# Performance work log

Measured on AMD Instinct MI355X. Metric: run time of the kernel, lower is better.

## Reference

```python
import jax, jax.numpy as jnp
import numpy as np

N_NODES = 100000
N_EDGES = 1600000
C_IN = 128
C_OUT = 64
BN_EPS = 1e-5
LEAKY_SLOPE = 0.01


def setup_inputs() -> dict:
    key = jax.random.key(0)
    k1, k2, k3 = jax.random.split(key, 3)
    x = jax.random.normal(k1, (N_NODES, C_IN), dtype=jnp.float32)
    edge_index = jax.random.randint(k2, (2, N_EDGES), 0, N_NODES, dtype=jnp.int32)
    W = jax.random.normal(k3, (C_IN, C_OUT), dtype=jnp.float32) * (1.0 / np.sqrt(C_IN))
    b = jnp.zeros((C_OUT,), dtype=jnp.float32)
    gamma = jnp.ones((C_OUT,), dtype=jnp.float32)
    beta = jnp.zeros((C_OUT,), dtype=jnp.float32)
    return {"x": x, "edge_index": edge_index, "W": W, "b": b, "gamma": gamma, "beta": beta}


def reference(x, edge_index, W, b, gamma, beta):
    n = x.shape[0]
    # --- GCNConv: add self-loops, symmetric normalization ---
    loop = jnp.arange(n, dtype=edge_index.dtype)
    row = jnp.concatenate([edge_index[0], loop])  # source
    col = jnp.concatenate([edge_index[1], loop])  # target
    deg = jax.ops.segment_sum(jnp.ones_like(col, dtype=x.dtype), col, num_segments=n)
    deg_inv_sqrt = jnp.where(deg > 0, jax.lax.rsqrt(deg), 0.0)
    norm = deg_inv_sqrt[row] * deg_inv_sqrt[col]  # [E+N]
    xw = x @ W  # [N, C_OUT] - transform before aggregation (PyG GCNConv)
    msgs = xw[row] * norm[:, None]  # [E+N, C_OUT]
    out = jax.ops.segment_sum(msgs, col, num_segments=n) + b  # [N, C_OUT]
    # --- BatchNorm (training mode: batch stats over nodes, biased var) ---
    mean = jnp.mean(out, axis=0)
    var = jnp.mean(jnp.square(out - mean), axis=0)
    y = gamma * (out - mean) * jax.lax.rsqrt(var + BN_EPS) + beta
    # --- LeakyReLU (default negative_slope=0.01); dropout p=0 is identity ---
    return jnp.where(y >= 0, y, LEAKY_SLOPE * y)
```

## Files before the change

### kernel.cpp

```cpp
#include <hip/hip_runtime.h>

#define C_IN 128
#define C_OUT 64
#define BN_EPS 1e-5f
#define LEAKY 0.01f

#define BSZ   256
#define NBMAX 512
#define CAP   6144
#define CHUNKA 2048

using bf16x8 = __attribute__((ext_vector_type(8))) __bf16;
using f32x4  = __attribute__((ext_vector_type(4))) float;

__device__ inline unsigned short f2b(float f) {
    unsigned u = __float_as_uint(f);
    return (unsigned short)((u + 0x7fffu + ((u >> 16) & 1u)) >> 16);
}
__device__ inline float b2f(unsigned short b) {
    return __uint_as_float(((unsigned)b) << 16);
}

__global__ __launch_bounds__(256) void k_prep(const float* __restrict__ W,
                                              unsigned short* __restrict__ wb,
                                              int* __restrict__ bfill,
                                              float* __restrict__ stats) {
    int idx = blockIdx.x * 256 + threadIdx.x;
    if (idx < NBMAX) bfill[idx] = 0;
    if (idx >= NBMAX && idx < NBMAX + 2 * C_OUT) stats[idx - NBMAX] = 0.f;
    if (idx >= C_IN * C_OUT) return;
    int k = idx >> 6, col = idx & 63;
    int t = col >> 4, nlo = col & 15;
    int c = k >> 5, q = (k >> 3) & 3, j = k & 7;
    wb[(size_t)((((t * 4 + c) * 4 + q) * 16) + nlo) * 8 + j] = f2b(W[idx]);
}

__global__ __launch_bounds__(256) void k_binA(const int* __restrict__ rows,
                                              const int* __restrict__ cols,
                                              int* __restrict__ bfill,
                                              unsigned* __restrict__ pairs,
                                              int nE, int NB) {
    __shared__ int hist[NBMAX];
    __shared__ int base[NBMAX];
    __shared__ int lstart[NBMAX];
    __shared__ int cursor[NBMAX];
    __shared__ unsigned lpair[CHUNKA];
    __shared__ unsigned short lbkt[CHUNKA];
    __shared__ unsigned lsorted[CHUNKA];
    __shared__ unsigned short lsbkt[CHUNKA];
    int t = threadIdx.x;
    int chunk = blockIdx.x * CHUNKA;
    int cnt = min(chunk + CHUNKA, nE) - chunk;

    hist[t] = 0; hist[t + 256] = 0;
    __syncthreads();

    for (int i = t; i < cnt; i += 256) {
        int c = cols[chunk + i];
        unsigned r = (unsigned)rows[chunk + i];
        int b = c >> 8;
        lpair[i] = ((unsigned)(c & (BSZ - 1)) << 24) | r;
        lbkt[i] = (unsigned short)b;
        atomicAdd(&hist[b], 1);
    }
    __syncthreads();

    int h0 = hist[t], h1 = hist[t + 256];
    if (t < NB && h0) base[t] = atomicAdd(&bfill[t], h0);
    if (t + 256 < NB && h1) base[t + 256] = atomicAdd(&bfill[t + 256], h1);
    lstart[t] = h0; lstart[t + 256] = h1;
    __syncthreads();
    for (int off = 1; off < 512; off <<= 1) {
        int a = (t >= off) ? lstart[t - off] : 0;
        int bb = lstart[t + 256 - off];
        __syncthreads();
        lstart[t] += a; lstart[t + 256] += bb;
        __syncthreads();
    }
    int s0 = lstart[t] - h0, s1 = lstart[t + 256] - h1;
    lstart[t] = s0; lstart[t + 256] = s1;
    cursor[t] = s0; cursor[t + 256] = s1;
    __syncthreads();

    for (int i = t; i < cnt; i += 256) {
        int b = lbkt[i];
        int pos = atomicAdd(&cursor[b], 1);
        lsorted[pos] = lpair[i];
        lsbkt[pos] = (unsigned short)b;
    }
    __syncthreads();

    for (int i = t; i < cnt; i += 256) {
        int b = lsbkt[i];
        int off = base[b] + (i - lstart[b]);
        if (off < CAP)
            pairs[(size_t)b * CAP + off] = lsorted[i];
    }
}

__global__ __launch_bounds__(256) void k_binB(const int* __restrict__ bfill,
                                              const unsigned* __restrict__ pairs,
                                              int2* __restrict__ pd,
                                              int* __restrict__ srcs, int n) {
    __shared__ unsigned rowbuf[CAP];
    __shared__ int sorted[CAP];
    __shared__ int histL[BSZ];
    __shared__ int scanL[BSZ];
    int b = blockIdx.x;
    int t = threadIdx.x;
    int cnt = min(bfill[b], CAP);
    const unsigned* reg = pairs + (size_t)b * CAP;

    histL[t] = 0;
    __syncthreads();
    for (int i = t; i < cnt; i += 256) {
        unsigned p = reg[i];
        rowbuf[i] = p;
        atomicAdd(&histL[p >> 24], 1);
    }
    __syncthreads();

    int hv = histL[t];
    scanL[t] = hv;
    __syncthreads();
    for (int off = 1; off < 256; off <<= 1) {
        int x = (t >= off) ? scanL[t - off] : 0;
        __syncthreads();
        scanL[t] += x;
        __syncthreads();
    }
    int my_start = scanL[t] - hv;

    int s0 = b * CAP;
    int node = (b << 8) + t;
    if (node < n) pd[node] = make_int2(s0 + my_start, hv);
    __syncthreads();
    histL[t] = my_start;
    __syncthreads();
    for (int i = t; i < cnt; i += 256) {
        unsigned p = rowbuf[i];
        int pos = atomicAdd(&histL[p >> 24], 1);
        sorted[pos] = (int)(p & 0xFFFFFFu);
    }
    __syncthreads();
    for (int i = t; i < cnt; i += 256)
        srcs[s0 + i] = sorted[i];
}

__global__ __launch_bounds__(256) void k_gemm(const float* __restrict__ x,
                                              const unsigned short* __restrict__ wb,
                                              const int2* __restrict__ pd,
                                              unsigned short* __restrict__ xwsb, int n) {
    const int lane = threadIdx.x & 63;
    const int wave = threadIdx.x >> 6;
    const int base = (blockIdx.x * 4 + wave) * 16;
    if (base >= n) return;

    const int nlo  = lane & 15;
    const int quad = lane >> 4;

    const bf16x8* Wv = (const bf16x8*)wb;
    bf16x8 Bf[4][4];
    #pragma unroll
    for (int t = 0; t < 4; ++t)
        #pragma unroll
        for (int c = 0; c < 4; ++c)
            Bf[t][c] = Wv[((t * 4 + c) * 4 + quad) * 16 + nlo];

    f32x4 acc[4] = {};
    int m = base + nlo;
    const float* xrow = x + (size_t)(m < n ? m : n - 1) * C_IN;

    #pragma unroll
    for (int c = 0; c < 4; ++c) {
        float4 a0 = *(const float4*)&xrow[c * 32 + quad * 8];
        float4 a1 = *(const float4*)&xrow[c * 32 + quad * 8 + 4];
        bf16x8 Af;
        Af[0] = (__bf16)a0.x; Af[1] = (__bf16)a0.y;
        Af[2] = (__bf16)a0.z; Af[3] = (__bf16)a0.w;
        Af[4] = (__bf16)a1.x; Af[5] = (__bf16)a1.y;
        Af[6] = (__bf16)a1.z; Af[7] = (__bf16)a1.w;
        #pragma unroll
        for (int t = 0; t < 4; ++t)
            acc[t] = __builtin_amdgcn_mfma_f32_16x16x32_bf16(Af, Bf[t][c], acc[t], 0, 0, 0);
    }

    #pragma unroll
    for (int r = 0; r < 4; ++r) {
        int node = base + quad * 4 + r;
        if (node < n) {
            float dn = rsqrtf((float)(pd[node].y + 1));
            #pragma unroll
            for (int t = 0; t < 4; ++t)
                xwsb[(size_t)node * C_OUT + t * 16 + nlo] = f2b(acc[t][r] * dn);
        }
    }
}

#define ACC8(d) do { \
    acc[0] += __uint_as_float((d).x << 16); \
    acc[1] += __uint_as_float((d).x & 0xffff0000u); \
    acc[2] += __uint_as_float((d).y << 16); \
    acc[3] += __uint_as_float((d).y & 0xffff0000u); \
    acc[4] += __uint_as_float((d).z << 16); \
    acc[5] += __uint_as_float((d).z & 0xffff0000u); \
    acc[6] += __uint_as_float((d).w << 16); \
    acc[7] += __uint_as_float((d).w & 0xffff0000u); } while (0)

__global__ __launch_bounds__(256) void k_gather(const int2* __restrict__ pd,
                                                const int* __restrict__ srcs,
                                                const unsigned short* __restrict__ xwsb,
                                                float* __restrict__ out, int n) {
    int lane = threadIdx.x & 63;
    int wv   = threadIdx.x >> 6;
    int s    = lane & 7;
    int g    = (lane >> 3) & 3;
    int h    = lane >> 5;
    int l32  = lane & 31;
    int c0 = s * 8 + ((lane & 8) ? 4 : 0) + ((lane & 16) ? 2 : 0);
    const uint4* xw16 = (const uint4*)xwsb;

    int node = blockIdx.x * 8 + wv * 2 + h;
    bool active = node < n;

    int2 p = active ? pd[node] : make_int2(0, 0);
    int dg = p.y;
    float dn = rsqrtf((float)(dg + 1));
    unsigned selfu = active ? *(const unsigned*)&xwsb[(size_t)node * C_OUT + c0] : 0u;

    float acc[8] = {0.f, 0.f, 0.f, 0.f, 0.f, 0.f, 0.f, 0.f};

    int sv = (active && l32 < dg) ? srcs[p.x + l32] : 0;
    for (int b2 = 0;;) {
        int m = dg - b2;
        #pragma unroll
        for (int j = 0; j < 8; ++j) {
            int idx = j * 4 + g;
            int src = __shfl(sv, (h << 5) + idx);
            if (idx < m) {
                uint4 d = xw16[((size_t)src << 3) + s];
                ACC8(d);
            }
        }
        b2 += 32;
        if (b2 >= dg) break;
        sv = (l32 < dg - b2) ? srcs[p.x + b2 + l32] : 0;
    }

    #pragma unroll
    for (int k = 0; k < 4; ++k) {
        float send = (lane & 8) ? acc[k] : acc[k + 4];
        float recv = __shfl_xor(send, 8);
        acc[k] = ((lane & 8) ? acc[k + 4] : acc[k]) + recv;
    }
    #pragma unroll
    for (int k = 0; k < 2; ++k) {
        float send = (lane & 16) ? acc[k] : acc[k + 2];
        float recv = __shfl_xor(send, 16);
        acc[k] = ((lane & 16) ? acc[k + 2] : acc[k]) + recv;
    }

    if (active) {
        float v0 = (acc[0] + __uint_as_float(selfu << 16)) * dn;
        float v1 = (acc[1] + __uint_as_float(selfu & 0xffff0000u)) * dn;
        *(float2*)&out[(size_t)node * C_OUT + c0] = make_float2(v0, v1);
    }
}

__global__ __launch_bounds__(256) void k_stats(const float* __restrict__ agg,
                                               float* __restrict__ stats, int n) {
    int c = threadIdx.x & 63;
    int sub = threadIdx.x >> 6;
    float s = 0.f, s2 = 0.f;
    for (int node = blockIdx.x * 4 + sub; node < n; node += gridDim.x * 4) {
        float v = agg[(size_t)node * C_OUT + c];
        s += v;
        s2 += v * v;
    }
    __shared__ float red[2][4][64];
    red[0][sub][c] = s;
    red[1][sub][c] = s2;
    __syncthreads();
    if (sub == 0) {
        s  = red[0][0][c] + red[0][1][c] + red[0][2][c] + red[0][3][c];
        s2 = red[1][0][c] + red[1][1][c] + red[1][2][c] + red[1][3][c];
        atomicAdd(&stats[c], s);
        atomicAdd(&stats[64 + c], s2);
    }
}

__global__ __launch_bounds__(256) void k_final(const float* __restrict__ stats,
                                               const float* __restrict__ gamma,
                                               const float* __restrict__ beta,
                                               float* __restrict__ out, int n) {
    int gid = blockIdx.x * 256 + threadIdx.x;
    int total4 = n * (C_OUT / 4);
    if (gid >= total4) return;
    int c4 = (gid & 15) * 4;
    float inv_n = 1.0f / (float)n;
    float4 s  = *(const float4*)&stats[c4];
    float4 s2 = *(const float4*)&stats[64 + c4];
    float4 g4 = *(const float4*)&gamma[c4];
    float4 b4 = *(const float4*)&beta[c4];
    float4 v = ((const float4*)out)[gid];

    float m, var, k, y;
    m = s.x * inv_n; var = s2.x * inv_n - m * m; k = rsqrtf(var + BN_EPS) * g4.x;
    y = (v.x - m) * k + b4.x; v.x = y >= 0.f ? y : LEAKY * y;
    m = s.y * inv_n; var = s2.y * inv_n - m * m; k = rsqrtf(var + BN_EPS) * g4.y;
    y = (v.y - m) * k + b4.y; v.y = y >= 0.f ? y : LEAKY * y;
    m = s.z * inv_n; var = s2.z * inv_n - m * m; k = rsqrtf(var + BN_EPS) * g4.z;
    y = (v.z - m) * k + b4.z; v.z = y >= 0.f ? y : LEAKY * y;
    m = s.w * inv_n; var = s2.w * inv_n - m * m; k = rsqrtf(var + BN_EPS) * g4.w;
    y = (v.w - m) * k + b4.w; v.w = y >= 0.f ? y : LEAKY * y;

    ((float4*)out)[gid] = v;
}

extern "C" void kernel_launch(void* const* d_in, const int* in_sizes, int n_in,
                              void* d_out, int out_size, void* d_ws, size_t ws_size,
                              hipStream_t stream) {
    const float* x     = (const float*)d_in[0];
    const int*   ei    = (const int*)d_in[1];
    const float* W     = (const float*)d_in[2];
    const float* gamma = (const float*)d_in[4];
    const float* beta  = (const float*)d_in[5];
    float* out = (float*)d_out;

    int n  = in_sizes[0] / C_IN;
    int nE = in_sizes[1] / 2;
    const int* rows = ei;
    const int* cols = ei + nE;
    int NB = (n + BSZ - 1) / BSZ;

    int2* pd = (int2*)d_ws;
    unsigned short* xwsb = (unsigned short*)(pd + n);
    unsigned* pairs = (unsigned*)(xwsb + (size_t)n * C_OUT);
    int* srcs = (int*)pairs;
    int* bfill = (int*)(pairs + (size_t)NB * CAP);
    float* stats = (float*)(bfill + NBMAX);
    unsigned short* wb = (unsigned short*)(stats + 2 * C_OUT);

    k_prep<<<(C_IN * C_OUT + 255) / 256, 256, 0, stream>>>(W, wb, bfill, stats);
    k_binA<<<(nE + CHUNKA - 1) / CHUNKA, 256, 0, stream>>>(rows, cols, bfill, pairs, nE, NB);
    k_binB<<<NB, 256, 0, stream>>>(bfill, pairs, pd, srcs, n);
    k_gemm<<<(n + 63) / 64, 256, 0, stream>>>(x, wb, pd, xwsb, n);
    k_gather<<<(n + 7) / 8, 256, 0, stream>>>(pd, srcs, xwsb, out, n);
    k_stats<<<512, 256, 0, stream>>>(out, stats, n);
    k_final<<<(n * (C_OUT / 4) + 255) / 256, 256, 0, stream>>>(stats, gamma, beta, out, n);
}
```

Measured before the change: 216.6 us.

## Fuse BatchNorm statistics into gather and use 16 lanes per node

```diff
diff --git a/kernel.cpp b/kernel.cpp
--- a/kernel.cpp
+++ b/kernel.cpp
@@ -9,6 +9,7 @@
 #define NBMAX 512
 #define CAP   6144
 #define CHUNKA 2048
+#define NPART 16
 
 using bf16x8 = __attribute__((ext_vector_type(8))) __bf16;
 using f32x4  = __attribute__((ext_vector_type(4))) float;
@@ -24,10 +25,10 @@
 __global__ __launch_bounds__(256) void k_prep(const float* __restrict__ W,
                                               unsigned short* __restrict__ wb,
                                               int* __restrict__ bfill,
-                                              float* __restrict__ stats) {
+                                              float* __restrict__ part) {
     int idx = blockIdx.x * 256 + threadIdx.x;
     if (idx < NBMAX) bfill[idx] = 0;
-    if (idx >= NBMAX && idx < NBMAX + 2 * C_OUT) stats[idx - NBMAX] = 0.f;
+    if (idx < NPART * 128) part[idx] = 0.f;
     if (idx >= C_IN * C_OUT) return;
     int k = idx >> 6, col = idx & 63;
     int t = col >> 4, nlo = col & 15;
@@ -210,41 +211,45 @@
 __global__ __launch_bounds__(256) void k_gather(const int2* __restrict__ pd,
                                                 const int* __restrict__ srcs,
                                                 const unsigned short* __restrict__ xwsb,
-                                                float* __restrict__ out, int n) {
+                                                float* __restrict__ out,
+                                                float* __restrict__ part, int n) {
+    __shared__ float sredS[16][64];
+    __shared__ float sredQ[16][64];
     int lane = threadIdx.x & 63;
     int wv   = threadIdx.x >> 6;
     int s    = lane & 7;
-    int g    = (lane >> 3) & 3;
-    int h    = lane >> 5;
-    int l32  = lane & 31;
-    int c0 = s * 8 + ((lane & 8) ? 4 : 0) + ((lane & 16) ? 2 : 0);
+    int g    = (lane >> 3) & 1;
+    int q    = lane >> 4;
+    int l16  = lane & 15;
+    int c0 = s * 8 + ((lane & 8) ? 4 : 0);
     const uint4* xw16 = (const uint4*)xwsb;
 
-    int node = blockIdx.x * 8 + wv * 2 + h;
+    int node = blockIdx.x * 16 + wv * 4 + q;
     bool active = node < n;
 
     int2 p = active ? pd[node] : make_int2(0, 0);
     int dg = p.y;
     float dn = rsqrtf((float)(dg + 1));
-    unsigned selfu = active ? *(const unsigned*)&xwsb[(size_t)node * C_OUT + c0] : 0u;
+    uint2 selfu = active ? *(const uint2*)&xwsb[(size_t)node * C_OUT + c0]
+                         : make_uint2(0u, 0u);
 
     float acc[8] = {0.f, 0.f, 0.f, 0.f, 0.f, 0.f, 0.f, 0.f};
 
-    int sv = (active && l32 < dg) ? srcs[p.x + l32] : 0;
+    int sv = (active && l16 < dg) ? srcs[p.x + l16] : 0;
     for (int b2 = 0;;) {
         int m = dg - b2;
         #pragma unroll
         for (int j = 0; j < 8; ++j) {
-            int idx = j * 4 + g;
-            int src = __shfl(sv, (h << 5) + idx);
+            int idx = j * 2 + g;
+            int src = __shfl(sv, (lane & 48) + idx);
             if (idx < m) {
                 uint4 d = xw16[((size_t)src << 3) + s];
                 ACC8(d);
             }
         }
-        b2 += 32;
+        b2 += 16;
         if (b2 >= dg) break;
-        sv = (l32 < dg - b2) ? srcs[p.x + b2 + l32] : 0;
+        sv = (l16 < dg - b2) ? srcs[p.x + b2 + l16] : 0;
     }
 
     #pragma unroll
@@ -253,65 +258,76 @@
         float recv = __shfl_xor(send, 8);
         acc[k] = ((lane & 8) ? acc[k + 4] : acc[k]) + recv;
     }
-    #pragma unroll
-    for (int k = 0; k < 2; ++k) {
-        float send = (lane & 16) ? acc[k] : acc[k + 2];
-        float recv = __shfl_xor(send, 16);
-        acc[k] = ((lane & 16) ? acc[k + 2] : acc[k]) + recv;
-    }
-
-    if (active) {
-        float v0 = (acc[0] + __uint_as_float(selfu << 16)) * dn;
-        float v1 = (acc[1] + __uint_as_float(selfu & 0xffff0000u)) * dn;
-        *(float2*)&out[(size_t)node * C_OUT + c0] = make_float2(v0, v1);
-    }
-}
-
-__global__ __launch_bounds__(256) void k_stats(const float* __restrict__ agg,
-                                               float* __restrict__ stats, int n) {
-    int c = threadIdx.x & 63;
-    int sub = threadIdx.x >> 6;
-    float s = 0.f, s2 = 0.f;
-    for (int node = blockIdx.x * 4 + sub; node < n; node += gridDim.x * 4) {
-        float v = agg[(size_t)node * C_OUT + c];
-        s += v;
-        s2 += v * v;
-    }
-    __shared__ float red[2][4][64];
-    red[0][sub][c] = s;
-    red[1][sub][c] = s2;
-    __syncthreads();
-    if (sub == 0) {
-        s  = red[0][0][c] + red[0][1][c] + red[0][2][c] + red[0][3][c];
-        s2 = red[1][0][c] + red[1][1][c] + red[1][2][c] + red[1][3][c];
-        atomicAdd(&stats[c], s);
-        atomicAdd(&stats[64 + c], s2);
-    }
-}
-
-__global__ __launch_bounds__(256) void k_final(const float* __restrict__ stats,
+
+    float v0 = active ? (acc[0] + __uint_as_float(selfu.x << 16)) * dn : 0.f;
+    float v1 = active ? (acc[1] + __uint_as_float(selfu.x & 0xffff0000u)) * dn : 0.f;
+    float v2 = active ? (acc[2] + __uint_as_float(selfu.y << 16)) * dn : 0.f;
+    float v3 = active ? (acc[3] + __uint_as_float(selfu.y & 0xffff0000u)) * dn : 0.f;
+
+    if (active)
+        *(float4*)&out[(size_t)node * C_OUT + c0] = make_float4(v0, v1, v2, v3);
+
+    int slot = wv * 4 + q;
+    sredS[slot][c0 + 0] = v0;       sredQ[slot][c0 + 0] = v0 * v0;
+    sredS[slot][c0 + 1] = v1;       sredQ[slot][c0 + 1] = v1 * v1;
+    sredS[slot][c0 + 2] = v2;       sredQ[slot][c0 + 2] = v2 * v2;
+    sredS[slot][c0 + 3] = v3;       sredQ[slot][c0 + 3] = v3 * v3;
+    __syncthreads();
+    int t = threadIdx.x;
+    if (t < 128) {
+        int cc = t & 63;
+        float a = 0.f;
+        if (t < 64) {
+            #pragma unroll
+            for (int j = 0; j < 16; ++j) a += sredS[j][cc];
+        } else {
+            #pragma unroll
+            for (int j = 0; j < 16; ++j) a += sredQ[j][cc];
+        }
+        atomicAdd(&part[(blockIdx.x & (NPART - 1)) * 128 + t], a);
+    }
+}
+
+__global__ __launch_bounds__(256) void k_final(const float* __restrict__ part,
                                                const float* __restrict__ gamma,
                                                const float* __restrict__ beta,
                                                float* __restrict__ out, int n) {
-    int gid = blockIdx.x * 256 + threadIdx.x;
+    __shared__ float lp[NPART * 128];
+    __shared__ float tot[128];
+    int t = threadIdx.x;
+    #pragma unroll
+    for (int r = 0; r < NPART * 128 / 256; ++r)
+        lp[t + r * 256] = part[t + r * 256];
+    __syncthreads();
+    if (t < 128) {
+        float a = 0.f;
+        #pragma unroll
+        for (int j = 0; j < NPART; ++j) a += lp[j * 128 + t];
+        tot[t] = a;
+    }
+    __syncthreads();
+
+    int gid = blockIdx.x * 256 + t;
     int total4 = n * (C_OUT / 4);
     if (gid >= total4) return;
     int c4 = (gid & 15) * 4;
     float inv_n = 1.0f / (float)n;
-    float4 s  = *(const float4*)&stats[c4];
-    float4 s2 = *(const float4*)&stats[64 + c4];
     float4 g4 = *(const float4*)&gamma[c4];
     float4 b4 = *(const float4*)&beta[c4];
     float4 v = ((const float4*)out)[gid];
 
     float m, var, k, y;
-    m = s.x * inv_n; var = s2.x * inv_n - m * m; k = rsqrtf(var + BN_EPS) * g4.x;
+    m = tot[c4 + 0] * inv_n; var = tot[64 + c4 + 0] * inv_n - m * m;
+    k = rsqrtf(var + BN_EPS) * g4.x;
     y = (v.x - m) * k + b4.x; v.x = y >= 0.f ? y : LEAKY * y;
-    m = s.y * inv_n; var = s2.y * inv_n - m * m; k = rsqrtf(var + BN_EPS) * g4.y;
+    m = tot[c4 + 1] * inv_n; var = tot[64 + c4 + 1] * inv_n - m * m;
+    k = rsqrtf(var + BN_EPS) * g4.y;
     y = (v.y - m) * k + b4.y; v.y = y >= 0.f ? y : LEAKY * y;
-    m = s.z * inv_n; var = s2.z * inv_n - m * m; k = rsqrtf(var + BN_EPS) * g4.z;
+    m = tot[c4 + 2] * inv_n; var = tot[64 + c4 + 2] * inv_n - m * m;
+    k = rsqrtf(var + BN_EPS) * g4.z;
     y = (v.z - m) * k + b4.z; v.z = y >= 0.f ? y : LEAKY * y;
-    m = s.w * inv_n; var = s2.w * inv_n - m * m; k = rsqrtf(var + BN_EPS) * g4.w;
+    m = tot[c4 + 3] * inv_n; var = tot[64 + c4 + 3] * inv_n - m * m;
+    k = rsqrtf(var + BN_EPS) * g4.w;
     y = (v.w - m) * k + b4.w; v.w = y >= 0.f ? y : LEAKY * y;
 
     ((float4*)out)[gid] = v;
@@ -338,14 +354,13 @@
     unsigned* pairs = (unsigned*)(xwsb + (size_t)n * C_OUT);
     int* srcs = (int*)pairs;
     int* bfill = (int*)(pairs + (size_t)NB * CAP);
-    float* stats = (float*)(bfill + NBMAX);
-    unsigned short* wb = (unsigned short*)(stats + 2 * C_OUT);
-
-    k_prep<<<(C_IN * C_OUT + 255) / 256, 256, 0, stream>>>(W, wb, bfill, stats);
+    float* part = (float*)(bfill + NBMAX);
+    unsigned short* wb = (unsigned short*)(part + NPART * 128);
+
+    k_prep<<<(C_IN * C_OUT + 255) / 256, 256, 0, stream>>>(W, wb, bfill, part);
     k_binA<<<(nE + CHUNKA - 1) / CHUNKA, 256, 0, stream>>>(rows, cols, bfill, pairs, nE, NB);
     k_binB<<<NB, 256, 0, stream>>>(bfill, pairs, pd, srcs, n);
     k_gemm<<<(n + 63) / 64, 256, 0, stream>>>(x, wb, pd, xwsb, n);
-    k_gather<<<(n + 7) / 8, 256, 0, stream>>>(pd, srcs, xwsb, out, n);
-    k_stats<<<512, 256, 0, stream>>>(out, stats, n);
-    k_final<<<(n * (C_OUT / 4) + 255) / 256, 256, 0, stream>>>(stats, gamma, beta, out, n);
-}
+    k_gather<<<(n + 15) / 16, 256, 0, stream>>>(pd, srcs, xwsb, out, part, n);
+    k_final<<<(n * (C_OUT / 4) + 255) / 256, 256, 0, stream>>>(part, gamma, beta, out, n);
+}
```

Result: faster. 197.0 us (-9.1%).
